# Performance work log

Measured on AMD Instinct MI355X. Metric: run time of the kernel, lower is better.

## Reference

```python
import jax, jax.numpy as jnp
import numpy as np
import math

D = 512; NA = 128; NC = 256; NB = 128; BATCH = 4; H = 8
EA, EC, EB = 4, 6, 4
KA, KC, KB = 2, 1, 2
F = 4 * D  # expert_ff_mult * embed_dim
N_TOTAL = NA + NC + NB


def setup_inputs() -> dict:
    key = jax.random.key(0)
    ks = jax.random.split(key, 16)
    s = 0.02
    def nrm(k, shape, scale=s):
        return jax.random.normal(k, shape, dtype=jnp.float32) * scale
    return {
        'tokens_A': jax.random.normal(ks[0], (BATCH, NA, D), dtype=jnp.float32),
        'tokens_B': jax.random.normal(ks[1], (BATCH, NB, D), dtype=jnp.float32),
        'tokens_C': jax.random.normal(ks[2], (BATCH, NC, D), dtype=jnp.float32),
        'ln1_g': jnp.ones((3, D), jnp.float32), 'ln1_b': jnp.zeros((3, D), jnp.float32),
        'ln2_g': jnp.ones((3, D), jnp.float32), 'ln2_b': jnp.zeros((3, D), jnp.float32),
        'Wqkv': nrm(ks[3], (3 * D, D)), 'bqkv': jnp.zeros((3 * D,), jnp.float32),
        'Wo': nrm(ks[4], (D, D)), 'bo': jnp.zeros((D,), jnp.float32),
        'Wr_A': nrm(ks[5], (D, EA)), 'br_A': jnp.zeros((EA,), jnp.float32),
        'W1_A': nrm(ks[6], (EA, D, F)), 'b1_A': jnp.zeros((EA, F), jnp.float32),
        'W2_A': nrm(ks[7], (EA, F, D)), 'b2_A': jnp.zeros((EA, D), jnp.float32),
        'Wr_C': nrm(ks[8], (D, EC)), 'br_C': jnp.zeros((EC,), jnp.float32),
        'W1_C': nrm(ks[9], (EC, D, F)), 'b1_C': jnp.zeros((EC, F), jnp.float32),
        'W2_C': nrm(ks[10], (EC, F, D)), 'b2_C': jnp.zeros((EC, D), jnp.float32),
        'Wr_B': nrm(ks[11], (D, EB)), 'br_B': jnp.zeros((EB,), jnp.float32),
        'W1_B': nrm(ks[12], (EB, D, F)), 'b1_B': jnp.zeros((EB, F), jnp.float32),
        'W2_B': nrm(ks[13], (EB, F, D)), 'b2_B': jnp.zeros((EB, D), jnp.float32),
    }


def _ln(x, g, b, eps=1e-5):
    m = jnp.mean(x, axis=-1, keepdims=True)
    v = jnp.var(x, axis=-1, keepdims=True)
    return (x - m) * jax.lax.rsqrt(v + eps) * g + b


def _directed_mask_bias():
    # segments: 0=A, 1=C, 2=B in [A|C|B] order; query may attend upstream groups only
    seg = jnp.concatenate([jnp.zeros(NA), jnp.ones(NC), 2.0 * jnp.ones(NB)])
    allowed = seg[None, :] <= seg[:, None]  # (N, N)
    return jnp.where(allowed, 0.0, -1e9).astype(jnp.float32)


def _mha(x, Wqkv, bqkv, Wo, bo, mask_bias):
    B, N, _ = x.shape
    qkv = x @ Wqkv.T + bqkv  # (B, N, 3D)
    q, k, v = jnp.split(qkv, 3, axis=-1)
    hd = D // H
    def heads(t):
        return t.reshape(B, N, H, hd).transpose(0, 2, 1, 3)  # (B, H, N, hd)
    q, k, v = heads(q), heads(k), heads(v)
    scores = jnp.einsum('bhqd,bhkd->bhqk', q, k) / math.sqrt(hd) + mask_bias[None, None]
    attn = jax.nn.softmax(scores, axis=-1)
    o = jnp.einsum('bhqk,bhkd->bhqd', attn, v).transpose(0, 2, 1, 3).reshape(B, N, D)
    return o @ Wo.T + bo


def _moe(x, Wr, br, W1, b1, W2, b2, k):
    # top-k routed expert FFN: softmax gates -> top-k renormalized -> dense combine
    probs = jax.nn.softmax(x @ Wr + br, axis=-1)  # (B, N, E)
    vals, idx = jax.lax.top_k(probs, k)
    vals = vals / jnp.sum(vals, axis=-1, keepdims=True)
    E = Wr.shape[1]
    gate = jnp.sum(jax.nn.one_hot(idx, E, dtype=x.dtype) * vals[..., None], axis=-2)  # (B, N, E)
    h = jax.nn.gelu(jnp.einsum('bnd,edf->benf', x, W1) + b1[None, :, None, :])
    y = jnp.einsum('benf,efd->bend', h, W2) + b2[None, :, None, :]
    return jnp.einsum('bne,bend->bnd', gate, y)


def reference(tokens_A, tokens_B, tokens_C, ln1_g, ln1_b, ln2_g, ln2_b,
              Wqkv, bqkv, Wo, bo,
              Wr_A, br_A, W1_A, b1_A, W2_A, b2_A,
              Wr_C, br_C, W1_C, b1_C, W2_C, b2_C,
              Wr_B, br_B, W1_B, b1_B, W2_B, b2_B):
    # 1-2. group-local pre-attention LN, concat [A | C | B]
    x = jnp.concatenate([
        _ln(tokens_A, ln1_g[0], ln1_b[0]),
        _ln(tokens_C, ln1_g[1], ln1_b[1]),
        _ln(tokens_B, ln1_g[2], ln1_b[2]),
    ], axis=1)
    # 3-4. shared directed self-attention + per-group residual
    attn = _mha(x, Wqkv, bqkv, Wo, bo, _directed_mask_bias())
    tA = tokens_A + attn[:, :NA]
    tC = tokens_C + attn[:, NA:NA + NC]
    tB = tokens_B + attn[:, NA + NC:]
    # 5. group-local pre-expert LN
    nA = _ln(tA, ln2_g[0], ln2_b[0])
    nC = _ln(tC, ln2_g[1], ln2_b[1])
    nB = _ln(tB, ln2_g[2], ln2_b[2])
    # 6-9. route A and C first, then B; residual add per group
    tA = tA + _moe(nA, Wr_A, br_A, W1_A, b1_A, W2_A, b2_A, KA)
    tC = tC + _moe(nC, Wr_C, br_C, W1_C, b1_C, W2_C, b2_C, KC)
    tB = tB + _moe(nB, Wr_B, br_B, W1_B, b1_B, W2_B, b2_B, KB)
    return jnp.concatenate([tA, tC, tB], axis=1)  # (B, NA+NC+NB, D)
```

## Files before the change

kernel.cpp:

```cpp
#include <hip/hip_runtime.h>
#include <hip/hip_bf16.h>
#include <cstdint>

#define DEV __device__ __forceinline__

using f32x4  = __attribute__((ext_vector_type(4))) float;
using bf16x8 = __attribute__((ext_vector_type(8))) __bf16;

static constexpr int D_    = 512;
static constexpr int ROWS  = 2048;
static constexpr int F_    = 2048;
static constexpr int NEXP  = 14;
static constexpr int NENT  = 3072;

#if defined(__has_builtin)
#if __has_builtin(__builtin_amdgcn_global_load_lds)
#define HAS_GLL 1
#endif
#endif

DEV unsigned short f2bf(float f) {
  unsigned int u = __builtin_bit_cast(unsigned int, f);
  unsigned int r = u + 0x7FFFu + ((u >> 16) & 1u);
  return (unsigned short)(r >> 16);
}
DEV unsigned int pack2(float a, float b) {
  return (unsigned int)f2bf(a) | ((unsigned int)f2bf(b) << 16);
}
DEV float gelu_tanh(float x) {
  float x3 = x * x * x;
  return 0.5f * x * (1.0f + tanhf(0.7978845608028654f * (x + 0.044715f * x3)));
}
DEV int prefix_base(const int* cnt, int e) {
  int base = 0;
  for (int i = 0; i < e; ++i) base += cnt[i];
  return base;
}

struct Shared128 { unsigned short As[128][72]; unsigned short Bs[64][72]; };

DEV void gemm128(const unsigned short* arow, const float* B, int ldb, int bcol0, int K,
                 f32x4 (&acc)[2][4], Shared128& sh)
{
  const int tid = threadIdx.x;
  const int lane = tid & 63, w = tid >> 6;
  const int ai = tid >> 1, ah = tid & 1;
  const int bj = tid >> 2, bq = tid & 3;
  for (int k0 = 0; k0 < K; k0 += 64) {
    __syncthreads();
    {
      const uint4* src = reinterpret_cast<const uint4*>(arow + k0 + ah * 32);
      uint4 v0 = src[0], v1 = src[1], v2 = src[2], v3 = src[3];
      uint4* dst = reinterpret_cast<uint4*>(&sh.As[ai][ah * 32]);
      dst[0] = v0; dst[1] = v1; dst[2] = v2; dst[3] = v3;
    }
    {
      const float4* src = reinterpret_cast<const float4*>(B + (size_t)(bcol0 + bj) * ldb + k0 + bq * 16);
      unsigned int pk[8];
      #pragma unroll
      for (int u = 0; u < 4; ++u) {
        float4 f = src[u];
        pk[u * 2]     = pack2(f.x, f.y);
        pk[u * 2 + 1] = pack2(f.z, f.w);
      }
      uint4* dst = reinterpret_cast<uint4*>(&sh.Bs[bj][bq * 16]);
      dst[0] = make_uint4(pk[0], pk[1], pk[2], pk[3]);
      dst[1] = make_uint4(pk[4], pk[5], pk[6], pk[7]);
    }
    __syncthreads();
    #pragma unroll
    for (int ks = 0; ks < 2; ++ks) {
      bf16x8 a[2], b[4];
      #pragma unroll
      for (int mi = 0; mi < 2; ++mi)
        a[mi] = *reinterpret_cast<const bf16x8*>(&sh.As[w * 32 + mi * 16 + (lane & 15)][ks * 32 + (lane >> 4) * 8]);
      #pragma unroll
      for (int ni = 0; ni < 4; ++ni)
        b[ni] = *reinterpret_cast<const bf16x8*>(&sh.Bs[ni * 16 + (lane & 15)][ks * 32 + (lane >> 4) * 8]);
      #pragma unroll
      for (int mi = 0; mi < 2; ++mi)
        #pragma unroll
        for (int ni = 0; ni < 4; ++ni)
          acc[mi][ni] = __builtin_amdgcn_mfma_f32_16x16x32_bf16(a[mi], b[ni], acc[mi][ni], 0, 0, 0);
    }
  }
}

struct __align__(16) SharedMoE { unsigned short As[64][72]; unsigned short Bs[8192]; };

DEV void gemm64x128L(const unsigned short* arow, const unsigned short* Bt,
                     f32x4 (&acc)[8], SharedMoE& sh)
{
  const int tid = threadIdx.x;
  const int lane = tid & 63, w = tid >> 6;
  const int ar = tid >> 2, aq = tid & 3;
  #pragma unroll
  for (int kt = 0; kt < 8; ++kt) {
    __syncthreads();
#ifdef HAS_GLL
    {
      const unsigned short* src = Bt + kt * 8192 + w * 2048 + lane * 8;
      unsigned short* dstBase = &sh.Bs[w * 2048];
      #pragma unroll
      for (int i = 0; i < 4; ++i)
        __builtin_amdgcn_global_load_lds(
            (const __attribute__((address_space(1))) unsigned int*)(src + i * 512),
            (__attribute__((address_space(3))) unsigned int*)(dstBase + i * 512),
            16, 0, 0);
    }
#else
    {
      const uint4* srcB = reinterpret_cast<const uint4*>(Bt + kt * 8192 + tid * 32);
      uint4 b0 = srcB[0], b1 = srcB[1], b2 = srcB[2], b3 = srcB[3];
      uint4* dstB = reinterpret_cast<uint4*>(&sh.Bs[tid * 32]);
      dstB[0] = b0; dstB[1] = b1; dstB[2] = b2; dstB[3] = b3;
    }
#endif
    {
      const uint4* srcA = reinterpret_cast<const uint4*>(arow + kt * 64 + aq * 16);
      uint4 a0 = srcA[0], a1 = srcA[1];
      uint4* dstA = reinterpret_cast<uint4*>(&sh.As[ar][aq * 16]);
      dstA[0] = a0; dstA[1] = a1;
    }
    __syncthreads();
    bf16x8 a0 = *reinterpret_cast<const bf16x8*>(&sh.As[w * 16 + (lane & 15)][0 * 32 + (lane >> 4) * 8]);
    bf16x8 a1 = *reinterpret_cast<const bf16x8*>(&sh.As[w * 16 + (lane & 15)][1 * 32 + (lane >> 4) * 8]);
    #pragma unroll
    for (int ni = 0; ni < 8; ++ni) {
      bf16x8 b0 = *reinterpret_cast<const bf16x8*>(&sh.Bs[(ni * 2 + 0) * 512 + lane * 8]);
      bf16x8 b1 = *reinterpret_cast<const bf16x8*>(&sh.Bs[(ni * 2 + 1) * 512 + lane * 8]);
      acc[ni] = __builtin_amdgcn_mfma_f32_16x16x32_bf16(a0, b0, acc[ni], 0, 0, 0);
      acc[ni] = __builtin_amdgcn_mfma_f32_16x16x32_bf16(a1, b1, acc[ni], 0, 0, 0);
    }
  }
}

DEV void pack_body(int pbid, int tid, unsigned short (*sh)[138],
                   const float* w1A, const float* w1C, const float* w1B,
                   const float* w2A, const float* w2C, const float* w2B,
                   unsigned short* W1P, unsigned short* W2P)
{
  int bx = pbid & 127, z = pbid >> 7;
  const float* src;
  unsigned short* dstbase;
  int ld, ntile, ktile, KT;
  if (z < 14) {
    int e = z;
    src = e < 4 ? w1A + (size_t)e * D_ * F_ : e < 10 ? w1C + (size_t)(e - 4) * D_ * F_ : w1B + (size_t)(e - 10) * D_ * F_;
    dstbase = W1P + (size_t)e * F_ * D_;
    ld = F_; KT = 8;
    ntile = bx >> 3; ktile = bx & 7;
  } else {
    int e = z - 14;
    src = e < 4 ? w2A + (size_t)e * F_ * D_ : e < 10 ? w2C + (size_t)(e - 4) * F_ * D_ : w2B + (size_t)(e - 10) * F_ * D_;
    dstbase = W2P + (size_t)e * D_ * F_;
    ld = D_; KT = 32;
    ntile = bx >> 5; ktile = bx & 31;
  }
  int k0 = ktile * 64, n0 = ntile * 128;
  {
    int r = tid >> 2, q = tid & 3;
    const float4* sp = reinterpret_cast<const float4*>(src + (size_t)(k0 + r) * ld + n0 + q * 32);
    unsigned int* shw = reinterpret_cast<unsigned int*>(&sh[r][q * 32]);
    #pragma unroll
    for (int u = 0; u < 8; ++u) {
      float4 v = sp[u];
      shw[u * 2]     = pack2(v.x, v.y);
      shw[u * 2 + 1] = pack2(v.z, v.w);
    }
  }
  __syncthreads();
  size_t tbase = (size_t)(ntile * KT + ktile) * 8192;
  #pragma unroll
  for (int i = 0; i < 4; ++i) {
    int p = tid + 256 * i;
    int f = p >> 6, l = p & 63;
    int ks = f & 1, ni = f >> 1;
    int nl = ni * 16 + (l & 15);
    int kl = ks * 32 + (l >> 4) * 8;
    unsigned short tmp[8];
    #pragma unroll
    for (int j = 0; j < 8; ++j) tmp[j] = sh[kl + j][nl];
    *reinterpret_cast<uint4*>(dstbase + tbase + (size_t)p * 8) = *reinterpret_cast<const uint4*>(tmp);
  }
}

__global__ __launch_bounds__(256) void k_ln(
    const float* tA, const float* tC, const float* tB,
    const float* g3, const float* b3, unsigned short* out)
{
  int r = blockIdx.x;
  int b = r >> 9, n = r & 511;
  int grp = n < 128 ? 0 : (n < 384 ? 1 : 2);
  const float* src = grp == 0 ? tA + (size_t)(b * 128 + n) * D_
                   : grp == 1 ? tC + (size_t)(b * 256 + n - 128) * D_
                              : tB + (size_t)(b * 128 + n - 384) * D_;
  int tid = threadIdx.x, lane = tid & 63, w = tid >> 6;
  float2 v = *reinterpret_cast<const float2*>(src + tid * 2);
  float s = v.x + v.y;
  float ss = v.x * v.x + v.y * v.y;
  #pragma unroll
  for (int off = 1; off < 64; off <<= 1) { s += __shfl_xor(s, off); ss += __shfl_xor(ss, off); }
  __shared__ float red[8];
  if (lane == 0) { red[w] = s; red[4 + w] = ss; }
  __syncthreads();
  float S  = red[0] + red[1] + red[2] + red[3];
  float SS = red[4] + red[5] + red[6] + red[7];
  float mean = S * (1.0f / 512.0f);
  float var  = SS * (1.0f / 512.0f) - mean * mean;
  float inv  = rsqrtf(var + 1e-5f);
  const float* gam = g3 + grp * D_;
  const float* bet = b3 + grp * D_;
  int d0 = tid * 2;
  out[(size_t)r * D_ + d0]     = f2bf((v.x - mean) * inv * gam[d0]     + bet[d0]);
  out[(size_t)r * D_ + d0 + 1] = f2bf((v.y - mean) * inv * gam[d0 + 1] + bet[d0 + 1]);
}

__global__ __launch_bounds__(256) void k_qkv_pack(
    const unsigned short* x, const float* Wqkv, const float* bqkv,
    unsigned short* Qg, unsigned short* Kg, unsigned short* Vg,
    const float* w1A, const float* w1C, const float* w1B,
    const float* w2A, const float* w2C, const float* w2B,
    unsigned short* W1P, unsigned short* W2P)
{
  __shared__ __align__(16) char smem[sizeof(Shared128)];
  int bid = blockIdx.x;
  int tid = threadIdx.x;
  if (bid < 384) {
    Shared128& sh = *reinterpret_cast<Shared128*>(smem);
    int bn = bid % 24, bm = (bid / 24) % 4, batch = bid / 96;
    int lane = tid & 63, w = tid >> 6;
    const unsigned short* arow = x + (size_t)(batch * 512 + bm * 128 + (tid >> 1)) * D_;
    f32x4 acc[2][4] = {};
    gemm128(arow, Wqkv, 512, bn * 64, 512, acc, sh);
    #pragma unroll
    for (int mi = 0; mi < 2; ++mi)
    #pragma unroll
    for (int ni = 0; ni < 4; ++ni)
    #pragma unroll
    for (int j = 0; j < 4; ++j) {
      int n = bm * 128 + w * 32 + mi * 16 + ((lane >> 4) << 2) + j;
      int col = bn * 64 + ni * 16 + (lane & 15);
      float val = acc[mi][ni][j] + bqkv[col];
      int part = col >> 9;
      int o = col & 511, h = o >> 6, d = o & 63;
      unsigned short* dst = part == 0 ? Qg : (part == 1 ? Kg : Vg);
      dst[(size_t)((batch * 8 + h) * 512 + n) * 64 + d] = f2bf(val);
    }
  } else {
    pack_body(bid - 384, tid, reinterpret_cast<unsigned short (*)[138]>(smem),
              w1A, w1C, w1B, w2A, w2C, w2B, W1P, W2P);
  }
}

__global__ __launch_bounds__(64) void k_attn(const unsigned short* Qg, const unsigned short* Kg,
                                             const unsigned short* Vg, unsigned short* attn)
{
  __shared__ unsigned short Qs[16][72], Ks[64][72], VT[64][72], Ps[16][72];
  int qt16 = blockIdx.x, h = blockIdx.y, b = blockIdx.z;
  int lane = threadIdx.x;
  const unsigned short* Qb  = Qg + (size_t)((b * 8 + h) * 512) * 64;
  const unsigned short* Kbp = Kg + (size_t)((b * 8 + h) * 512) * 64;
  const unsigned short* Vbp = Vg + (size_t)((b * 8 + h) * 512) * 64;
  int q0 = qt16 * 16;
  {
    int row = lane >> 2, q4 = lane & 3;
    const uint4* src = reinterpret_cast<const uint4*>(Qb + (size_t)(q0 + row) * 64 + q4 * 16);
    uint4* dst = reinterpret_cast<uint4*>(&Qs[row][q4 * 16]);
    dst[0] = src[0]; dst[1] = src[1];
  }
  int nkt = qt16 < 8 ? 2 : (qt16 < 24 ? 6 : 8);
  float mrun[4] = { -1e30f, -1e30f, -1e30f, -1e30f };
  float lrun[4] = {};
  f32x4 o[4] = {};
  for (int kt = 0; kt < nkt; ++kt) {
    #pragma unroll
    for (int it = 0; it < 4; ++it) {
      int row = it * 16 + (lane >> 2), q4 = lane & 3;
      const uint4* ksrc = reinterpret_cast<const uint4*>(Kbp + (size_t)(kt * 64 + row) * 64 + q4 * 16);
      uint4* kdst = reinterpret_cast<uint4*>(&Ks[row][q4 * 16]);
      kdst[0] = ksrc[0]; kdst[1] = ksrc[1];
      union { uint4 u; unsigned short s[8]; } vv0, vv1;
      const uint4* vsrc = reinterpret_cast<const uint4*>(Vbp + (size_t)(kt * 64 + row) * 64 + q4 * 16);
      vv0.u = vsrc[0]; vv1.u = vsrc[1];
      #pragma unroll
      for (int jj = 0; jj < 8; ++jj) {
        VT[q4 * 16 + jj][row]     = vv0.s[jj];
        VT[q4 * 16 + 8 + jj][row] = vv1.s[jj];
      }
    }
    f32x4 s[4] = {};
    #pragma unroll
    for (int ks = 0; ks < 2; ++ks) {
      bf16x8 aq = *reinterpret_cast<const bf16x8*>(&Qs[lane & 15][ks * 32 + (lane >> 4) * 8]);
      #pragma unroll
      for (int cc = 0; cc < 4; ++cc) {
        bf16x8 bk = *reinterpret_cast<const bf16x8*>(&Ks[cc * 16 + (lane & 15)][ks * 32 + (lane >> 4) * 8]);
        s[cc] = __builtin_amdgcn_mfma_f32_16x16x32_bf16(aq, bk, s[cc], 0, 0, 0);
      }
    }
    #pragma unroll
    for (int rr = 0; rr < 4; ++rr) {
      float s0 = s[0][rr] * 0.125f, s1 = s[1][rr] * 0.125f;
      float s2 = s[2][rr] * 0.125f, s3 = s[3][rr] * 0.125f;
      float mx = fmaxf(fmaxf(s0, s1), fmaxf(s2, s3));
      #pragma unroll
      for (int off = 1; off < 16; off <<= 1) mx = fmaxf(mx, __shfl_xor(mx, off));
      float mn = fmaxf(mrun[rr], mx);
      float al = expf(mrun[rr] - mn);
      mrun[rr] = mn;
      float p0 = expf(s0 - mn), p1 = expf(s1 - mn), p2 = expf(s2 - mn), p3 = expf(s3 - mn);
      float ps = p0 + p1 + p2 + p3;
      #pragma unroll
      for (int off = 1; off < 16; off <<= 1) ps += __shfl_xor(ps, off);
      lrun[rr] = lrun[rr] * al + ps;
      #pragma unroll
      for (int n4 = 0; n4 < 4; ++n4) o[n4][rr] *= al;
      int prow = ((lane >> 4) << 2) + rr;
      Ps[prow][0 * 16 + (lane & 15)] = f2bf(p0);
      Ps[prow][1 * 16 + (lane & 15)] = f2bf(p1);
      Ps[prow][2 * 16 + (lane & 15)] = f2bf(p2);
      Ps[prow][3 * 16 + (lane & 15)] = f2bf(p3);
    }
    #pragma unroll
    for (int ks = 0; ks < 2; ++ks) {
      bf16x8 ap = *reinterpret_cast<const bf16x8*>(&Ps[lane & 15][ks * 32 + (lane >> 4) * 8]);
      #pragma unroll
      for (int n4 = 0; n4 < 4; ++n4) {
        bf16x8 bv = *reinterpret_cast<const bf16x8*>(&VT[n4 * 16 + (lane & 15)][ks * 32 + (lane >> 4) * 8]);
        o[n4] = __builtin_amdgcn_mfma_f32_16x16x32_bf16(ap, bv, o[n4], 0, 0, 0);
      }
    }
  }
  #pragma unroll
  for (int n4 = 0; n4 < 4; ++n4)
  #pragma unroll
  for (int rr = 0; rr < 4; ++rr) {
    int qrow = q0 + ((lane >> 4) << 2) + rr;
    int col = h * 64 + n4 * 16 + (lane & 15);
    float val = o[n4][rr] / lrun[rr];
    attn[(size_t)(b * 512 + qrow) * 512 + col] = f2bf(val);
  }
}

__global__ __launch_bounds__(256) void k_wo_pack(
    const unsigned short* attn, const float* Wo, const float* bo,
    const float* tokA, const float* tokC, const float* tokB, float* out,
    const float* w1A, const float* w1C, const float* w1B,
    const float* w2A, const float* w2C, const float* w2B,
    unsigned short* W1P, unsigned short* W2P)
{
  __shared__ __align__(16) char smem[sizeof(Shared128)];
  int bid = blockIdx.x;
  int tid = threadIdx.x;
  if (bid < 128) {
    Shared128& sh = *reinterpret_cast<Shared128*>(smem);
    int bn = bid & 7, bm = bid >> 3;
    int lane = tid & 63, w = tid >> 6;
    const unsigned short* arow = attn + (size_t)(bm * 128 + (tid >> 1)) * D_;
    f32x4 acc[2][4] = {};
    gemm128(arow, Wo, 512, bn * 64, 512, acc, sh);
    #pragma unroll
    for (int mi = 0; mi < 2; ++mi)
    #pragma unroll
    for (int ni = 0; ni < 4; ++ni)
    #pragma unroll
    for (int j = 0; j < 4; ++j) {
      int row = bm * 128 + w * 32 + mi * 16 + ((lane >> 4) << 2) + j;
      int col = bn * 64 + ni * 16 + (lane & 15);
      float val = acc[mi][ni][j] + bo[col];
      int b = row >> 9, n = row & 511;
      float res;
      if (n < 128)      res = tokA[(size_t)(b * 128 + n) * D_ + col];
      else if (n < 384) res = tokC[(size_t)(b * 256 + n - 128) * D_ + col];
      else              res = tokB[(size_t)(b * 128 + n - 384) * D_ + col];
      out[(size_t)row * D_ + col] = res + val;
    }
  } else {
    pack_body(1200 + bid - 128, tid, reinterpret_cast<unsigned short (*)[138]>(smem),
              w1A, w1C, w1B, w2A, w2C, w2B, W1P, W2P);
  }
}

__global__ __launch_bounds__(256) void k_router_pack(const float* t,
    const float* ln2g, const float* ln2b,
    const float* WrA, const float* brA, const float* WrC, const float* brC,
    const float* WrB, const float* brB,
    int* cnt, int* tokexp, float* tokgate, unsigned short* nrm,
    const float* w1A, const float* w1C, const float* w1B,
    const float* w2A, const float* w2C, const float* w2B,
    unsigned short* W1P, unsigned short* W2P)
{
  __shared__ __align__(16) char smem[64 * 138 * 2];
  int bid = blockIdx.x;
  if (bid >= 512) {
    pack_body(2400 + bid - 512, threadIdx.x, reinterpret_cast<unsigned short (*)[138]>(smem),
              w1A, w1C, w1B, w2A, w2C, w2B, W1P, W2P);
    return;
  }
  int w = threadIdx.x >> 6, lane = threadIdx.x & 63;
  int r = bid * 4 + w;
  int n = r & 511;
  int grp = n < 128 ? 0 : (n < 384 ? 1 : 2);
  int E = grp == 1 ? 6 : 4;
  int topk = grp == 1 ? 1 : 2;
  int egbase = grp == 0 ? 0 : (grp == 1 ? 4 : 10);
  const float* Wr = grp == 0 ? WrA : (grp == 1 ? WrC : WrB);
  const float* br = grp == 0 ? brA : (grp == 1 ? brC : brB);
  const float* tr = t + (size_t)r * D_;
  float xv[8];
  float s = 0.0f, ss = 0.0f;
  #pragma unroll
  for (int it = 0; it < 8; ++it) {
    float v = tr[it * 64 + lane];
    xv[it] = v; s += v; ss += v * v;
  }
  #pragma unroll
  for (int off = 1; off < 64; off <<= 1) { s += __shfl_xor(s, off); ss += __shfl_xor(ss, off); }
  float mean = s * (1.0f / 512.0f);
  float var  = ss * (1.0f / 512.0f) - mean * mean;
  float inv  = rsqrtf(var + 1e-5f);
  const float* gam = ln2g + grp * D_;
  const float* bet = ln2b + grp * D_;
  float acc[6] = {};
  #pragma unroll
  for (int it = 0; it < 8; ++it) {
    int d = it * 64 + lane;
    float nv = (xv[it] - mean) * inv * gam[d] + bet[d];
    nrm[(size_t)r * D_ + d] = f2bf(nv);
    #pragma unroll
    for (int e = 0; e < 6; ++e) if (e < E) acc[e] += nv * Wr[d * E + e];
  }
  #pragma unroll
  for (int e = 0; e < 6; ++e)
    #pragma unroll
    for (int off = 1; off < 64; off <<= 1) acc[e] += __shfl_xor(acc[e], off);
  if (lane == 0) {
    float p[6];
    float mx = -1e30f;
    #pragma unroll
    for (int e = 0; e < 6; ++e) if (e < E) { p[e] = acc[e] + br[e]; mx = fmaxf(mx, p[e]); }
    float sum = 0.0f;
    #pragma unroll
    for (int e = 0; e < 6; ++e) if (e < E) { p[e] = expf(p[e] - mx); sum += p[e]; }
    #pragma unroll
    for (int e = 0; e < 6; ++e) if (e < E) p[e] /= sum;
    int i1 = 0; float v1 = p[0];
    #pragma unroll
    for (int e = 1; e < 6; ++e) if (e < E && p[e] > v1) { v1 = p[e]; i1 = e; }
    if (topk == 1) {
      tokexp[r * 2]     = egbase + i1; tokgate[r * 2]     = 1.0f;
      tokexp[r * 2 + 1] = -1;          tokgate[r * 2 + 1] = 0.0f;
      atomicAdd(&cnt[egbase + i1], 1);
    } else {
      int i2 = -1; float v2 = -1e30f;
      #pragma unroll
      for (int e = 0; e < 6; ++e) if (e < E && e != i1 && p[e] > v2) { v2 = p[e]; i2 = e; }
      float tot = v1 + v2;
      tokexp[r * 2]     = egbase + i1; tokgate[r * 2]     = v1 / tot;
      tokexp[r * 2 + 1] = egbase + i2; tokgate[r * 2 + 1] = v2 / tot;
      atomicAdd(&cnt[egbase + i1], 1);
      atomicAdd(&cnt[egbase + i2], 1);
    }
  }
}

__global__ __launch_bounds__(256) void k_scatter(const int* tokexp, const float* tokgate,
                                                 const int* cnt, int* cursor, int* list, float* gate)
{
  int r = blockIdx.x * 256 + threadIdx.x;
  #pragma unroll
  for (int j = 0; j < 2; ++j) {
    int e = tokexp[r * 2 + j];
    if (e >= 0) {
      int base = prefix_base(cnt, e);
      int s = atomicAdd(&cursor[e], 1);
      list[base + s] = r;
      gate[base + s] = tokgate[r * 2 + j];
    }
  }
}

__global__ __launch_bounds__(256) void k_moe1(const unsigned short* nrm, const unsigned short* W1P,
    const float* b1A, const float* b1C, const float* b1B,
    const int* cnt, const int* list, unsigned short* H)
{
  int ft = blockIdx.x, tt = blockIdx.y, e = blockIdx.z;
  int c = cnt[e];
  if (tt * 64 >= c) return;
  __shared__ SharedMoE sh;
  const float* b1 = e < 4 ? b1A + (size_t)e * F_ : e < 10 ? b1C + (size_t)(e - 4) * F_ : b1B + (size_t)(e - 10) * F_;
  const unsigned short* Bt = W1P + (size_t)e * F_ * D_ + (size_t)(ft * 8) * 8192;
  int base = prefix_base(cnt, e);
  int tid = threadIdx.x, lane = tid & 63, w = tid >> 6;
  int ig = tt * 64 + (tid >> 2);
  int tok = list[base + (ig < c ? ig : c - 1)];
  const unsigned short* arow = nrm + (size_t)tok * D_;
  f32x4 acc[8] = {};
  gemm64x128L(arow, Bt, acc, sh);
  #pragma unroll
  for (int ni = 0; ni < 8; ++ni)
  #pragma unroll
  for (int j = 0; j < 4; ++j) {
    int rl = w * 16 + ((lane >> 4) << 2) + j;
    int sg = tt * 64 + rl;
    if (sg < c) {
      int col = ft * 128 + ni * 16 + (lane & 15);
      float val = acc[ni][j] + b1[col];
      H[(size_t)(base + sg) * F_ + col] = f2bf(gelu_tanh(val));
    }
  }
}

__global__ __launch_bounds__(256) void k_moe2(const unsigned short* H, const unsigned short* W2P,
    const float* b2A, const float* b2C, const float* b2B,
    const int* cnt, const int* list, const float* gate, float* out)
{
  int dt = blockIdx.x, tt = blockIdx.y >> 2, kc = blockIdx.y & 3, e = blockIdx.z;
  int c = cnt[e];
  if (tt * 64 >= c) return;
  __shared__ SharedMoE sh;
  const float* b2 = e < 4 ? b2A + (size_t)e * D_ : e < 10 ? b2C + (size_t)(e - 4) * D_ : b2B + (size_t)(e - 10) * D_;
  const unsigned short* Bt = W2P + (size_t)e * D_ * F_ + (size_t)(dt * 32 + kc * 8) * 8192;
  int base = prefix_base(cnt, e);
  int tid = threadIdx.x, lane = tid & 63, w = tid >> 6;
  int ig = tt * 64 + (tid >> 2);
  const unsigned short* arow = H + (size_t)(base + (ig < c ? ig : c - 1)) * F_ + kc * 512;
  f32x4 acc[8] = {};
  gemm64x128L(arow, Bt, acc, sh);
  #pragma unroll
  for (int ni = 0; ni < 8; ++ni)
  #pragma unroll
  for (int j = 0; j < 4; ++j) {
    int rl = w * 16 + ((lane >> 4) << 2) + j;
    int sg = tt * 64 + rl;
    if (sg < c) {
      int col = dt * 128 + ni * 16 + (lane & 15);
      float val = acc[ni][j] + (kc == 0 ? b2[col] : 0.0f);
      int tok = list[base + sg];
      atomicAdd(&out[(size_t)tok * D_ + col], gate[base + sg] * val);
    }
  }
}

extern "C" void kernel_launch(void* const* d_in, const int* in_sizes, int n_in,
                              void* d_out, int out_size, void* d_ws, size_t ws_size,
                              hipStream_t stream)
{
  const float* tokA = (const float*)d_in[0];
  const float* tokB = (const float*)d_in[1];
  const float* tokC = (const float*)d_in[2];
  const float* ln1g = (const float*)d_in[3];
  const float* ln1b = (const float*)d_in[4];
  const float* ln2g = (const float*)d_in[5];
  const float* ln2b = (const float*)d_in[6];
  const float* Wqkv = (const float*)d_in[7];
  const float* bqkv = (const float*)d_in[8];
  const float* Wo   = (const float*)d_in[9];
  const float* bo   = (const float*)d_in[10];
  const float* WrA  = (const float*)d_in[11];
  const float* brA  = (const float*)d_in[12];
  const float* W1A  = (const float*)d_in[13];
  const float* b1A  = (const float*)d_in[14];
  const float* W2A  = (const float*)d_in[15];
  const float* b2A  = (const float*)d_in[16];
  const float* WrC  = (const float*)d_in[17];
  const float* brC  = (const float*)d_in[18];
  const float* W1C  = (const float*)d_in[19];
  const float* b1C  = (const float*)d_in[20];
  const float* W2C  = (const float*)d_in[21];
  const float* b2C  = (const float*)d_in[22];
  const float* WrB  = (const float*)d_in[23];
  const float* brB  = (const float*)d_in[24];
  const float* W1B  = (const float*)d_in[25];
  const float* b1B  = (const float*)d_in[26];
  const float* W2B  = (const float*)d_in[27];
  const float* b2B  = (const float*)d_in[28];
  float* out = (float*)d_out;

  char* ws = (char*)d_ws;
  const size_t MB = 1024 * 1024;
  const size_t WSTRIDE = (size_t)NEXP * F_ * D_ * 2;
  unsigned short* xb   = (unsigned short*)(ws);
  unsigned short* nrm  = xb;
  unsigned short* Qg   = (unsigned short*)(ws + 2 * MB);
  unsigned short* Kg   = (unsigned short*)(ws + 4 * MB);
  unsigned short* Vg   = (unsigned short*)(ws + 6 * MB);
  unsigned short* attn = (unsigned short*)(ws + 8 * MB);
  unsigned short* W1P  = (unsigned short*)(ws + 16 * MB);
  unsigned short* W2P  = (unsigned short*)(ws + 16 * MB + WSTRIDE);
  unsigned short* H    = (unsigned short*)(ws + 16 * MB + 2 * WSTRIDE);
  char* small = ws + 16 * MB + 2 * WSTRIDE + (size_t)NENT * F_ * 2;
  int*   cnt     = (int*)(small);
  int*   cursor  = (int*)(small + 64);
  int*   tokexp  = (int*)(small + 256);
  float* tokgate = (float*)(small + 256 + ROWS * 2 * 4);
  int*   list    = (int*)(small + 256 + ROWS * 4 * 4);
  float* gate    = (float*)(small + 256 + ROWS * 4 * 4 + NENT * 4);

  hipMemsetAsync(cnt, 0, 128, stream);
  k_ln<<<ROWS, 256, 0, stream>>>(tokA, tokC, tokB, ln1g, ln1b, xb);
  k_qkv_pack<<<384 + 1200, 256, 0, stream>>>(xb, Wqkv, bqkv, Qg, Kg, Vg,
                                             W1A, W1C, W1B, W2A, W2C, W2B, W1P, W2P);
  k_attn<<<dim3(32, 8, 4), 64, 0, stream>>>(Qg, Kg, Vg, attn);
  k_wo_pack<<<128 + 1200, 256, 0, stream>>>(attn, Wo, bo, tokA, tokC, tokB, out,
                                            W1A, W1C, W1B, W2A, W2C, W2B, W1P, W2P);
  k_router_pack<<<512 + 1184, 256, 0, stream>>>(out, ln2g, ln2b, WrA, brA, WrC, brC, WrB, brB,
                                                cnt, tokexp, tokgate, nrm,
                                                W1A, W1C, W1B, W2A, W2C, W2B, W1P, W2P);
  k_scatter<<<8, 256, 0, stream>>>(tokexp, tokgate, cnt, cursor, list, gate);
  k_moe1<<<dim3(16, 16, 14), 256, 0, stream>>>(nrm, W1P, b1A, b1C, b1B, cnt, list, H);
  k_moe2<<<dim3(4, 64, 14), 256, 0, stream>>>(H, W2P, b2A, b2C, b2B, cnt, list, gate, out);
}
```

Baseline: 207.0 us.

## Double MoE token tile per block and move W2 packing into moe1 kernel

The MoE GEMMs now process 128 tokens per block as two 64-row A tiles sharing each staged B (weight) tile, which halves weight reloads from global memory per token. The bf16 weight-packing work is redistributed: fewer pack blocks ride along with the QKV, Wo and router kernels, and the remaining blocks (the W2 portion) are appended to the moe1 launch. This trades occupancy and extra LDS and registers for less weight traffic. The moe1 weight reads depend on W1 packing having finished in earlier kernels, so ordering correctness rests on the new block offsets.

```diff
diff --git a/kernel.cpp b/kernel.cpp
--- a/kernel.cpp
+++ b/kernel.cpp
@@ -86,10 +86,10 @@
   }
 }
 
-struct __align__(16) SharedMoE { unsigned short As[64][72]; unsigned short Bs[8192]; };
-
-DEV void gemm64x128L(const unsigned short* arow, const unsigned short* Bt,
-                     f32x4 (&acc)[8], SharedMoE& sh)
+struct __align__(16) SharedMoE2 { unsigned short As[2][64][72]; unsigned short Bs[8192]; };
+
+DEV void gemm2x64x128(const unsigned short* arow0, const unsigned short* arow1,
+                      const unsigned short* Bt, f32x4 (&acc0)[8], f32x4 (&acc1)[8], SharedMoE2& sh)
 {
   const int tid = threadIdx.x;
   const int lane = tid & 63, w = tid >> 6;
@@ -117,20 +117,28 @@
     }
 #endif
     {
-      const uint4* srcA = reinterpret_cast<const uint4*>(arow + kt * 64 + aq * 16);
-      uint4 a0 = srcA[0], a1 = srcA[1];
-      uint4* dstA = reinterpret_cast<uint4*>(&sh.As[ar][aq * 16]);
-      dstA[0] = a0; dstA[1] = a1;
+      const uint4* s0 = reinterpret_cast<const uint4*>(arow0 + kt * 64 + aq * 16);
+      uint4 a0 = s0[0], a1 = s0[1];
+      uint4* d0 = reinterpret_cast<uint4*>(&sh.As[0][ar][aq * 16]);
+      d0[0] = a0; d0[1] = a1;
+      const uint4* s1 = reinterpret_cast<const uint4*>(arow1 + kt * 64 + aq * 16);
+      uint4 a2 = s1[0], a3 = s1[1];
+      uint4* d1 = reinterpret_cast<uint4*>(&sh.As[1][ar][aq * 16]);
+      d1[0] = a2; d1[1] = a3;
     }
     __syncthreads();
-    bf16x8 a0 = *reinterpret_cast<const bf16x8*>(&sh.As[w * 16 + (lane & 15)][0 * 32 + (lane >> 4) * 8]);
-    bf16x8 a1 = *reinterpret_cast<const bf16x8*>(&sh.As[w * 16 + (lane & 15)][1 * 32 + (lane >> 4) * 8]);
+    bf16x8 a00 = *reinterpret_cast<const bf16x8*>(&sh.As[0][w * 16 + (lane & 15)][0 * 32 + (lane >> 4) * 8]);
+    bf16x8 a01 = *reinterpret_cast<const bf16x8*>(&sh.As[0][w * 16 + (lane & 15)][1 * 32 + (lane >> 4) * 8]);
+    bf16x8 a10 = *reinterpret_cast<const bf16x8*>(&sh.As[1][w * 16 + (lane & 15)][0 * 32 + (lane >> 4) * 8]);
+    bf16x8 a11 = *reinterpret_cast<const bf16x8*>(&sh.As[1][w * 16 + (lane & 15)][1 * 32 + (lane >> 4) * 8]);
     #pragma unroll
     for (int ni = 0; ni < 8; ++ni) {
       bf16x8 b0 = *reinterpret_cast<const bf16x8*>(&sh.Bs[(ni * 2 + 0) * 512 + lane * 8]);
       bf16x8 b1 = *reinterpret_cast<const bf16x8*>(&sh.Bs[(ni * 2 + 1) * 512 + lane * 8]);
-      acc[ni] = __builtin_amdgcn_mfma_f32_16x16x32_bf16(a0, b0, acc[ni], 0, 0, 0);
-      acc[ni] = __builtin_amdgcn_mfma_f32_16x16x32_bf16(a1, b1, acc[ni], 0, 0, 0);
+      acc0[ni] = __builtin_amdgcn_mfma_f32_16x16x32_bf16(a00, b0, acc0[ni], 0, 0, 0);
+      acc0[ni] = __builtin_amdgcn_mfma_f32_16x16x32_bf16(a01, b1, acc0[ni], 0, 0, 0);
+      acc1[ni] = __builtin_amdgcn_mfma_f32_16x16x32_bf16(a10, b0, acc1[ni], 0, 0, 0);
+      acc1[ni] = __builtin_amdgcn_mfma_f32_16x16x32_bf16(a11, b1, acc1[ni], 0, 0, 0);
     }
   }
 }
@@ -377,7 +385,7 @@
       out[(size_t)row * D_ + col] = res + val;
     }
   } else {
-    pack_body(1200 + bid - 128, tid, reinterpret_cast<unsigned short (*)[138]>(smem),
+    pack_body(896 + bid - 128, tid, reinterpret_cast<unsigned short (*)[138]>(smem),
               w1A, w1C, w1B, w2A, w2C, w2B, W1P, W2P);
   }
 }
@@ -394,7 +402,7 @@
   __shared__ __align__(16) char smem[64 * 138 * 2];
   int bid = blockIdx.x;
   if (bid >= 512) {
-    pack_body(2400 + bid - 512, threadIdx.x, reinterpret_cast<unsigned short (*)[138]>(smem),
+    pack_body(1344 + bid - 512, threadIdx.x, reinterpret_cast<unsigned short (*)[138]>(smem),
               w1A, w1C, w1B, w2A, w2C, w2B, W1P, W2P);
     return;
   }
@@ -481,34 +489,46 @@
   }
 }
 
-__global__ __launch_bounds__(256) void k_moe1(const unsigned short* nrm, const unsigned short* W1P,
+__global__ __launch_bounds__(256) void k_moe1_pack(const unsigned short* nrm, const unsigned short* W1P,
     const float* b1A, const float* b1C, const float* b1B,
-    const int* cnt, const int* list, unsigned short* H)
-{
-  int ft = blockIdx.x, tt = blockIdx.y, e = blockIdx.z;
+    const int* cnt, const int* list, unsigned short* H,
+    const float* w1A, const float* w1C, const float* w1B,
+    const float* w2A, const float* w2C, const float* w2B,
+    unsigned short* W1Pd, unsigned short* W2P)
+{
+  __shared__ __align__(16) char smem[sizeof(SharedMoE2)];
+  int bid = blockIdx.x;
+  int tid = threadIdx.x;
+  if (bid >= 1792) {
+    pack_body(bid, tid, reinterpret_cast<unsigned short (*)[138]>(smem),
+              w1A, w1C, w1B, w2A, w2C, w2B, W1Pd, W2P);
+    return;
+  }
+  int e = bid >> 7, rem = bid & 127;
+  int ft = rem & 15, tt = rem >> 4;
   int c = cnt[e];
-  if (tt * 64 >= c) return;
-  __shared__ SharedMoE sh;
+  if (tt * 128 >= c) return;
+  SharedMoE2& sh = *reinterpret_cast<SharedMoE2*>(smem);
   const float* b1 = e < 4 ? b1A + (size_t)e * F_ : e < 10 ? b1C + (size_t)(e - 4) * F_ : b1B + (size_t)(e - 10) * F_;
   const unsigned short* Bt = W1P + (size_t)e * F_ * D_ + (size_t)(ft * 8) * 8192;
   int base = prefix_base(cnt, e);
-  int tid = threadIdx.x, lane = tid & 63, w = tid >> 6;
-  int ig = tt * 64 + (tid >> 2);
-  int tok = list[base + (ig < c ? ig : c - 1)];
-  const unsigned short* arow = nrm + (size_t)tok * D_;
-  f32x4 acc[8] = {};
-  gemm64x128L(arow, Bt, acc, sh);
+  int lane = tid & 63, w = tid >> 6;
+  int ig0 = tt * 128 + (tid >> 2);
+  int ig1 = ig0 + 64;
+  const unsigned short* arow0 = nrm + (size_t)list[base + (ig0 < c ? ig0 : c - 1)] * D_;
+  const unsigned short* arow1 = nrm + (size_t)list[base + (ig1 < c ? ig1 : c - 1)] * D_;
+  f32x4 acc0[8] = {}, acc1[8] = {};
+  gemm2x64x128(arow0, arow1, Bt, acc0, acc1, sh);
   #pragma unroll
   for (int ni = 0; ni < 8; ++ni)
   #pragma unroll
   for (int j = 0; j < 4; ++j) {
     int rl = w * 16 + ((lane >> 4) << 2) + j;
-    int sg = tt * 64 + rl;
-    if (sg < c) {
-      int col = ft * 128 + ni * 16 + (lane & 15);
-      float val = acc[ni][j] + b1[col];
-      H[(size_t)(base + sg) * F_ + col] = f2bf(gelu_tanh(val));
-    }
+    int col = ft * 128 + ni * 16 + (lane & 15);
+    int sg0 = tt * 128 + rl;
+    if (sg0 < c) H[(size_t)(base + sg0) * F_ + col] = f2bf(gelu_tanh(acc0[ni][j] + b1[col]));
+    int sg1 = sg0 + 64;
+    if (sg1 < c) H[(size_t)(base + sg1) * F_ + col] = f2bf(gelu_tanh(acc1[ni][j] + b1[col]));
   }
 }
 
@@ -516,29 +536,38 @@
     const float* b2A, const float* b2C, const float* b2B,
     const int* cnt, const int* list, const float* gate, float* out)
 {
-  int dt = blockIdx.x, tt = blockIdx.y >> 2, kc = blockIdx.y & 3, e = blockIdx.z;
+  int rem = blockIdx.x, e = blockIdx.y;
+  int dt = rem & 3, kc = (rem >> 2) & 3, tt = rem >> 4;
   int c = cnt[e];
-  if (tt * 64 >= c) return;
-  __shared__ SharedMoE sh;
+  if (tt * 128 >= c) return;
+  __shared__ __align__(16) char smem[sizeof(SharedMoE2)];
+  SharedMoE2& sh = *reinterpret_cast<SharedMoE2*>(smem);
   const float* b2 = e < 4 ? b2A + (size_t)e * D_ : e < 10 ? b2C + (size_t)(e - 4) * D_ : b2B + (size_t)(e - 10) * D_;
   const unsigned short* Bt = W2P + (size_t)e * D_ * F_ + (size_t)(dt * 32 + kc * 8) * 8192;
   int base = prefix_base(cnt, e);
   int tid = threadIdx.x, lane = tid & 63, w = tid >> 6;
-  int ig = tt * 64 + (tid >> 2);
-  const unsigned short* arow = H + (size_t)(base + (ig < c ? ig : c - 1)) * F_ + kc * 512;
-  f32x4 acc[8] = {};
-  gemm64x128L(arow, Bt, acc, sh);
+  int ig0 = tt * 128 + (tid >> 2);
+  int ig1 = ig0 + 64;
+  const unsigned short* arow0 = H + (size_t)(base + (ig0 < c ? ig0 : c - 1)) * F_ + kc * 512;
+  const unsigned short* arow1 = H + (size_t)(base + (ig1 < c ? ig1 : c - 1)) * F_ + kc * 512;
+  f32x4 acc0[8] = {}, acc1[8] = {};
+  gemm2x64x128(arow0, arow1, Bt, acc0, acc1, sh);
   #pragma unroll
   for (int ni = 0; ni < 8; ++ni)
   #pragma unroll
   for (int j = 0; j < 4; ++j) {
     int rl = w * 16 + ((lane >> 4) << 2) + j;
-    int sg = tt * 64 + rl;
-    if (sg < c) {
-      int col = dt * 128 + ni * 16 + (lane & 15);
-      float val = acc[ni][j] + (kc == 0 ? b2[col] : 0.0f);
-      int tok = list[base + sg];
-      atomicAdd(&out[(size_t)tok * D_ + col], gate[base + sg] * val);
+    int col = dt * 128 + ni * 16 + (lane & 15);
+    float bias = (kc == 0 ? b2[col] : 0.0f);
+    int sg0 = tt * 128 + rl;
+    if (sg0 < c) {
+      int tok = list[base + sg0];
+      atomicAdd(&out[(size_t)tok * D_ + col], gate[base + sg0] * (acc0[ni][j] + bias));
+    }
+    int sg1 = sg0 + 64;
+    if (sg1 < c) {
+      int tok = list[base + sg1];
+      atomicAdd(&out[(size_t)tok * D_ + col], gate[base + sg1] * (acc1[ni][j] + bias));
     }
   }
 }
@@ -600,15 +629,16 @@
 
   hipMemsetAsync(cnt, 0, 128, stream);
   k_ln<<<ROWS, 256, 0, stream>>>(tokA, tokC, tokB, ln1g, ln1b, xb);
-  k_qkv_pack<<<384 + 1200, 256, 0, stream>>>(xb, Wqkv, bqkv, Qg, Kg, Vg,
-                                             W1A, W1C, W1B, W2A, W2C, W2B, W1P, W2P);
+  k_qkv_pack<<<384 + 896, 256, 0, stream>>>(xb, Wqkv, bqkv, Qg, Kg, Vg,
+                                            W1A, W1C, W1B, W2A, W2C, W2B, W1P, W2P);
   k_attn<<<dim3(32, 8, 4), 64, 0, stream>>>(Qg, Kg, Vg, attn);
-  k_wo_pack<<<128 + 1200, 256, 0, stream>>>(attn, Wo, bo, tokA, tokC, tokB, out,
-                                            W1A, W1C, W1B, W2A, W2C, W2B, W1P, W2P);
-  k_router_pack<<<512 + 1184, 256, 0, stream>>>(out, ln2g, ln2b, WrA, brA, WrC, brC, WrB, brB,
-                                                cnt, tokexp, tokgate, nrm,
-                                                W1A, W1C, W1B, W2A, W2C, W2B, W1P, W2P);
+  k_wo_pack<<<128 + 448, 256, 0, stream>>>(attn, Wo, bo, tokA, tokC, tokB, out,
+                                           W1A, W1C, W1B, W2A, W2C, W2B, W1P, W2P);
+  k_router_pack<<<512 + 448, 256, 0, stream>>>(out, ln2g, ln2b, WrA, brA, WrC, brC, WrB, brB,
+                                               cnt, tokexp, tokgate, nrm,
+                                               W1A, W1C, W1B, W2A, W2C, W2B, W1P, W2P);
   k_scatter<<<8, 256, 0, stream>>>(tokexp, tokgate, cnt, cursor, list, gate);
-  k_moe1<<<dim3(16, 16, 14), 256, 0, stream>>>(nrm, W1P, b1A, b1C, b1B, cnt, list, H);
-  k_moe2<<<dim3(4, 64, 14), 256, 0, stream>>>(H, W2P, b2A, b2C, b2B, cnt, list, gate, out);
-}
+  k_moe1_pack<<<3584, 256, 0, stream>>>(nrm, W1P, b1A, b1C, b1B, cnt, list, H,
+                                        W1A, W1C, W1B, W2A, W2C, W2B, W1P, W2P);
+  k_moe2<<<dim3(128, 14), 256, 0, stream>>>(H, W2P, b2A, b2C, b2B, cnt, list, gate, out);
+}
```

Result: slower. 232.3 us (+12.3%).
